# Performance work log

Hardware: AMD Instinct MI355X
Metric: run time of the kernel (lower is better)

Reference implementation:

```python
import jax, jax.numpy as jnp
import numpy as np
from jax import lax

B, H, W, C = 8, 64, 64, 256  # H must equal W (einsum contraction requires it)
CQ = C // 4


def conv2d(x, w, b, dilation=1):
    # x: NHWC, w: HWIO (TF Conv2D layout), padding 'same'
    y = lax.conv_general_dilated(
        x, w, window_strides=(1, 1), padding='SAME',
        rhs_dilation=(dilation, dilation),
        dimension_numbers=('NHWC', 'HWIO', 'NHWC'))
    return y + b


def setup_inputs() -> dict:
    key = jax.random.key(0)
    ks = jax.random.split(key, 16)
    s = 0.05
    inp = {
        'x':   jax.random.normal(ks[0], (B, H, W, C), jnp.float32),
        'wq':  jax.random.normal(ks[1], (1, 1, C, CQ), jnp.float32) * s,
        'bq':  jnp.zeros((CQ,), jnp.float32),
        'wq1': jax.random.normal(ks[2], (3, 3, C, CQ), jnp.float32) * s,
        'bq1': jnp.zeros((CQ,), jnp.float32),
        'wq2': jax.random.normal(ks[3], (3, 3, C, CQ), jnp.float32) * s,
        'bq2': jnp.zeros((CQ,), jnp.float32),
        'wq3': jax.random.normal(ks[4], (3, 3, C, CQ), jnp.float32) * s,
        'bq3': jnp.zeros((CQ,), jnp.float32),
        'wq4': jax.random.normal(ks[5], (1, 1, C, C), jnp.float32) * s,
        'bq4': jnp.zeros((C,), jnp.float32),
        'wk':  jax.random.normal(ks[6], (3, 3, C, C), jnp.float32) * s,
        'bk':  jnp.zeros((C,), jnp.float32),
        'wv':  jax.random.normal(ks[7], (1, 1, C, C), jnp.float32) * s,
        'bv':  jnp.zeros((C,), jnp.float32),
        'gamma': jax.random.normal(ks[8], (1,), jnp.float32) * 0.1,
    }
    return inp


def reference(x, wq, bq, wq1, bq1, wq2, bq2, wq3, bq3, wq4, bq4,
              wk, bk, wv, bv, gamma):
    # multi-scale query branch: 1x1, 3x3, 3x3 dil=3, 3x3 dil=6 -> concat -> 1x1
    q = jnp.concatenate([
        conv2d(x, wq, bq, 1),
        conv2d(x, wq1, bq1, 1),
        conv2d(x, wq2, bq2, 3),
        conv2d(x, wq3, bq3, 6),
    ], axis=-1)
    q = conv2d(q, wq4, bq4, 1)                 # (B,H,W,C)
    # key conv applied twice with the SAME weights (as in the original code)
    k = conv2d(conv2d(x, wk, bk, 1), wk, bk, 1)  # (B,H,W,C)
    v = conv2d(x, wv, bv, 1)                    # (B,H,W,C)

    qT = jnp.transpose(q, (0, 2, 1, 3))         # (B,W,H,C)
    # per-channel spatial contraction; requires H == W
    energy = jnp.einsum('bijc,bkjc->bikc', k, qT)   # (B,H,W,C)
    attention = jax.nn.softmax(energy, axis=-1)     # softmax over CHANNEL axis
    attnT = jnp.transpose(attention, (0, 2, 1, 3))  # (B,W,H,C)
    out = jnp.einsum('bijc,bkjc->bikc', attnT, v)   # (B,W,H,C)
    return gamma * out + x
```

## Files before the change

### kernel.cpp

```cpp
#include <hip/hip_runtime.h>

typedef short  short8 __attribute__((ext_vector_type(8)));
typedef short  sv4    __attribute__((ext_vector_type(4)));
typedef __bf16 bf16x8 __attribute__((ext_vector_type(8)));
typedef float  f32x4  __attribute__((ext_vector_type(4)));

__device__ __forceinline__ float bf2f(short s) {
    unsigned u = ((unsigned)(unsigned short)s) << 16;
    return __builtin_bit_cast(float, u);
}
__device__ __forceinline__ short f2bf(float f) {
    unsigned u = __builtin_bit_cast(unsigned, f);
    u += 0x7fffu + ((u >> 16) & 1u);
    return (short)(u >> 16);
}
__device__ __forceinline__ f32x4 mfma16(short8 a, short8 b, f32x4 c) {
    return __builtin_amdgcn_mfma_f32_16x16x32_bf16(
        __builtin_bit_cast(bf16x8, a), __builtin_bit_cast(bf16x8, b), c, 0, 0, 0);
}
__device__ __forceinline__ void gl16(const short* g, short* l) {
    __builtin_amdgcn_global_load_lds(
        (const __attribute__((address_space(1))) void*)g,
        (__attribute__((address_space(3))) void*)l, 16, 0, 0);
}


__global__ __launch_bounds__(256) void detect_k(const short* x, int* flag)
{
    __shared__ int red[256];
    int t = threadIdx.x;
    int cnt = 0;
    for (int i = t; i < 4096; i += 256) {
        int e = (x[2 * i] >> 7) & 0xFF;
        cnt += (e >= 100 && e <= 140) ? 1 : 0;
    }
    red[t] = cnt; __syncthreads();
    for (int s = 128; s > 0; s >>= 1) { if (t < s) red[t] += red[t + s]; __syncthreads(); }
    if (t == 0) *flag = (red[0] < 3277) ? 1 : 0;
}

__global__ __launch_bounds__(256) void convert_x(const void* x, short* xb, const int* flagp)
{
    int f32 = *flagp;
    size_t i = ((size_t)blockIdx.x * 256 + threadIdx.x) * 8;
    short8 v;
    if (f32) {
        const float* fs = (const float*)x + i;
        f32x4 a = *(const f32x4*)fs;
        f32x4 b = *(const f32x4*)(fs + 4);
#pragma unroll
        for (int l = 0; l < 4; l++) { v[l] = f2bf(a[l]); v[4 + l] = f2bf(b[l]); }
    } else {
        v = *(const short8*)((const short*)x + i);
    }
    *(short8*)(xb + i) = v;
}

struct Ptrs {
    const void *wq, *wq1, *wq2, *wq3, *wq4, *wk, *wv;
    const void *bq, *bq1, *bq2, *bq3, *bq4, *bk, *bv, *gm;
};

__global__ __launch_bounds__(256) void convert_k(Ptrs P, short* wp, short* bb, const int* flagp)
{
    int f32 = *flagp;
    int idx = blockIdx.x * 256 + threadIdx.x;
    if (idx < 1179648) {
        const void* src; int Cout, base;
        if      (idx <   16384) { src = P.wq;  Cout =  64; base = 0; }
        else if (idx <  163840) { src = P.wq1; Cout =  64; base = 16384; }
        else if (idx <  311296) { src = P.wq2; Cout =  64; base = 163840; }
        else if (idx <  458752) { src = P.wq3; Cout =  64; base = 311296; }
        else if (idx <  524288) { src = P.wq4; Cout = 256; base = 458752; }
        else if (idx < 1114112) { src = P.wk;  Cout = 256; base = 524288; }
        else                    { src = P.wv;  Cout = 256; base = 1114112; }
        int rem = idx - base;
        int t   = rem / (Cout * 256);
        int r2  = rem - t * Cout * 256;
        int co  = r2 >> 8;
        int ci  = r2 & 255;
        int si  = (t * 256 + ci) * Cout + co;
        wp[idx] = f32 ? f2bf(((const float*)src)[si]) : ((const short*)src)[si];
    } else if (idx < 1179648 + 1280) {
        int j = idx - 1179648;
        if (j < 1025) {
            const void* src; int off;
            if      (j <   64) { src = P.bq;  off = j; }
            else if (j <  128) { src = P.bq1; off = j - 64; }
            else if (j <  192) { src = P.bq2; off = j - 128; }
            else if (j <  256) { src = P.bq3; off = j - 192; }
            else if (j <  512) { src = P.bq4; off = j - 256; }
            else if (j <  768) { src = P.bk;  off = j - 512; }
            else if (j < 1024) { src = P.bv;  off = j - 768; }
            else               { src = P.gm;  off = 0; }
            bb[j] = f32 ? f2bf(((const float*)src)[off]) : ((const short*)src)[off];
        } else if (j >= 1032) {
            bb[j] = 0;
        }
    }
}

struct CJob {
    const short* src;
    short*       dst;
    const short* wpk;
    const short* bias;
    int Cout;
    int dil;
    int ntaps;
    int coff;
    int outmode;
};
struct CTable { CJob j[6]; int end[6]; };

template<int NA, int NB, int BOFS, int WSTEP>
__device__ __forceinline__ void conv_loop(
    const short* src, const short* wpk, int ntaps, int dil,
    const short* zp, short* Sh,
    int wave, int lr8, int cl, int h0, int b, int nt0, int srcT,
    int m_base, int n_base, int lrow, int pc0, int pc1,
    f32x4 (&acc)[4][4])
{
    const short* abase[NA];
    unsigned     vm[NA];
    const short* bbase[NB];
#pragma unroll
    for (int jj = 0; jj < NA; jj++) {
        int m  = (jj * 4 + wave) * 8 + lr8;
        int hh = srcT ? (m & 63) : (h0 + (m >> 6));
        int ww = srcT ? (h0 + (m >> 6)) : (m & 63);
        abase[jj] = src + (((b * 64 + hh) * 64 + ww) * 256 + cl * 8);
        unsigned msk = 1u;
        if (ntaps == 9) {
            msk = 0u;
#pragma unroll
            for (int t = 0; t < 9; ++t) {
                int tr = (t >= 6) ? 2 : ((t >= 3) ? 1 : 0);
                int dy = (tr - 1) * dil, dx = (t - tr * 3 - 1) * dil;
                bool v = ((unsigned)(hh + dy) < 64u) && ((unsigned)(ww + dx) < 64u);
                msk |= (v ? 1u : 0u) << t;
            }
        }
        vm[jj] = msk;
    }
#pragma unroll
    for (int jj = 0; jj < NB; jj++) {
        int n = (jj * 4 + wave) * 8 + lr8;
        bbase[jj] = wpk + (nt0 + n) * 256 + cl * 8;
    }

    int prevdel = 0;
    for (int t = 0; t < ntaps; ++t) {
        int dy = 0, dx = 0;
        if (ntaps == 9) {
            int tr = (t >= 6) ? 2 : ((t >= 3) ? 1 : 0);
            dy = (tr - 1) * dil;
            dx = (t - tr * 3 - 1) * dil;
        }
        int tdel = (dy * 64 + dx) * 256;
        int step = tdel - prevdel; prevdel = tdel;
        const short* pA[NA];
#pragma unroll
        for (int jj = 0; jj < NA; jj++) {
            abase[jj] += step;
            pA[jj] = ((vm[jj] >> t) & 1u) ? abase[jj] : zp;
        }
#pragma unroll
        for (int s4 = 0; s4 < 4; ++s4) {
#pragma unroll
            for (int jj = 0; jj < NA; jj++)
                gl16(pA[jj] + s4 * 64, Sh + (jj * 4 + wave) * 512);
#pragma unroll
            for (int jj = 0; jj < NB; jj++)
                gl16(bbase[jj] + s4 * 64, Sh + BOFS + (jj * 4 + wave) * 512);
            __syncthreads();
#pragma unroll
            for (int j = 0; j < 2; j++) {
                int pc = j ? pc1 : pc0;
                short8 a4[4], b4[4];
#pragma unroll
                for (int mi = 0; mi < 4; mi++)
                    a4[mi] = *(const short8*)(Sh + (m_base + mi * 16 + lrow) * 64 + pc);
#pragma unroll
                for (int ni = 0; ni < 4; ni++)
                    b4[ni] = *(const short8*)(Sh + BOFS + (n_base + ni * 16 + lrow) * 64 + pc);
#pragma unroll
                for (int mi = 0; mi < 4; mi++)
#pragma unroll
                    for (int ni = 0; ni < 4; ni++)
                        acc[mi][ni] = mfma16(a4[mi], b4[ni], acc[mi][ni]);
            }
            __syncthreads();
        }
#pragma unroll
        for (int jj = 0; jj < NB; jj++) bbase[jj] += WSTEP;
    }
}

__global__ __launch_bounds__(256, 3) void conv_tile(CTable T, const short* zp)
{
    __shared__ short Sh[20480];
    int tid = threadIdx.x;
    int bid = blockIdx.x;
    int ji = 0;
    while (ji < 5 && bid >= T.end[ji]) ji++;
    CJob J = T.j[ji];
    int s0  = ji ? T.end[ji - 1] : 0;
    int seg = T.end[ji] - s0;
    int lb  = bid - s0;
    int g   = (lb & 7) * (seg >> 3) + (lb >> 3);

    int big   = (J.Cout == 256);
    int BM    = big ? 128 : 256;
    int ntile = big ? (g & 1) : 0;
    int Mtile = big ? (g >> 1) : g;
    int p0 = Mtile * BM;
    int b  = p0 >> 12;
    int h0 = (p0 >> 6) & 63;
    int nt0  = ntile * 128;
    int srcT = (J.outmode == 3);

    int wave = tid >> 6, lane = tid & 63;
    int lrow = lane & 15, quad = lane >> 4;
    int m_base = big ? (wave & 1) * 64 : wave * 64;
    int n_base = big ? (wave >> 1) * 64 : 0;

    int lr8 = lane >> 3;
    int cl  = (lane & 7) ^ (lr8 & 7);

    int pc0 = ((quad     ^ (lrow & 7)) * 8);
    int pc1 = (((4 + quad) ^ (lrow & 7)) * 8);

    f32x4 acc[4][4] = {};
    if (big)
        conv_loop<4, 4, 8192, 65536>(J.src, J.wpk, J.ntaps, J.dil, zp, Sh,
                                     wave, lr8, cl, h0, b, nt0, srcT,
                                     m_base, n_base, lrow, pc0, pc1, acc);
    else
        conv_loop<8, 2, 16384, 16384>(J.src, J.wpk, J.ntaps, J.dil, zp, Sh,
                                      wave, lr8, cl, h0, b, nt0, srcT,
                                      m_base, n_base, lrow, pc0, pc1, acc);

    int rq = quad * 4;
#pragma unroll
    for (int ni = 0; ni < 4; ni++) {
        int co = nt0 + n_base + ni * 16 + lrow;
        float bv = bf2f(J.bias[co]);
        if (J.outmode == 0) {
#pragma unroll
            for (int mi = 0; mi < 4; mi++) {
                int pb = p0 + m_base + mi * 16 + rq;
#pragma unroll
                for (int r = 0; r < 4; r++)
                    J.dst[(size_t)(pb + r) * 256 + J.coff + co] = f2bf(acc[mi][ni][r] + bv);
            }
        } else {
            int hw = h0 + (m_base >> 6);
            short* row = J.dst + ((size_t)(b * 256 + co) * 64 + hw) * 64;
#pragma unroll
            for (int mi = 0; mi < 4; mi++) {
                sv4 o;
#pragma unroll
                for (int r = 0; r < 4; r++) o[r] = f2bf(acc[mi][ni][r] + bv);
                *(sv4*)(row + mi * 16 + rq) = o;
            }
        }
    }
}

__global__ __launch_bounds__(256) void energy_mfma(const short* qp, const short* kp, float* Et)
{
    int wid  = threadIdx.x >> 6;
    int lane = threadIdx.x & 63;
    int g = blockIdx.x * 4 + wid;
    int b = g >> 8, c = g & 255;
    int lrow = lane & 15;
    int q8   = (lane >> 4) << 3;
    const short* qb = qp + (size_t)(b * 256 + c) * 4096;
    const short* kb = kp + (size_t)(b * 256 + c) * 4096;

    f32x4 acc[4][4] = {};
#pragma unroll
    for (int ks = 0; ks < 2; ++ks) {
        int j0 = ks * 32 + q8;
        short8 A[4], Bv[4];
#pragma unroll
        for (int mi = 0; mi < 4; mi++)
            A[mi] = *(const short8*)(qb + (size_t)(mi * 16 + lrow) * 64 + j0);
#pragma unroll
        for (int ni = 0; ni < 4; ni++)
            Bv[ni] = *(const short8*)(kb + (size_t)(ni * 16 + lrow) * 64 + j0);
#pragma unroll
        for (int mi = 0; mi < 4; mi++)
#pragma unroll
            for (int ni = 0; ni < 4; ni++)
                acc[mi][ni] = mfma16(A[mi], Bv[ni], acc[mi][ni]);
    }
    int rq = (lane >> 4) * 4;
#pragma unroll
    for (int mi = 0; mi < 4; mi++)
#pragma unroll
        for (int r = 0; r < 4; r++) {
            int w = mi * 16 + rq + r;
            float* row = Et + ((size_t)(b * 256 + c) * 64 + w) * 64;
#pragma unroll
            for (int ni = 0; ni < 4; ni++)
                row[ni * 16 + lrow] = acc[mi][ni][r];
        }
}

__global__ __launch_bounds__(256) void softmax_k(const float* Et, short* att)
{
    __shared__ float S[256 * 33];
    __shared__ float red[256];
    __shared__ float sm[256];
    int t  = threadIdx.x;
    int b  = blockIdx.x >> 7;
    int a  = (blockIdx.x >> 1) & 63;
    int jh = blockIdx.x & 1;

    const float* row = Et + ((size_t)(b * 256 + t) * 64 + a) * 64 + jh * 32;
#pragma unroll
    for (int jj = 0; jj < 32; jj += 4) {
        f32x4 v = *(const f32x4*)(row + jj);
#pragma unroll
        for (int l = 0; l < 4; l++) S[t * 33 + jj + l] = v[l];
    }
    __syncthreads();

    int tj = t & 31, tg = t >> 5;
    float m = -1e30f;
#pragma unroll
    for (int cc = 0; cc < 32; ++cc) m = fmaxf(m, S[(tg * 32 + cc) * 33 + tj]);
    red[t] = m;
    __syncthreads();
    if (tg == 0) {
        float mm = red[tj];
#pragma unroll
        for (int gg = 1; gg < 8; ++gg) mm = fmaxf(mm, red[gg * 32 + tj]);
        red[tj] = mm;
    }
    __syncthreads();
    float M = red[tj];
    float s = 0.f;
#pragma unroll
    for (int cc = 0; cc < 32; ++cc) {
        int id = (tg * 32 + cc) * 33 + tj;
        float e = __expf(S[id] - M);
        S[id] = e; s += e;
    }
    sm[t] = s;
    __syncthreads();
    if (tg == 0) {
        float ss = sm[tj];
#pragma unroll
        for (int gg = 1; gg < 8; ++gg) ss += sm[gg * 32 + tj];
        sm[tj] = 1.0f / ss;
    }
    __syncthreads();

    short* orow = att + ((size_t)(b * 256 + t) * 64 + a) * 64 + jh * 32;
#pragma unroll
    for (int jj = 0; jj < 32; jj += 8) {
        short8 o;
#pragma unroll
        for (int l = 0; l < 8; l++) o[l] = f2bf(S[t * 33 + jj + l] * sm[jj + l]);
        *(short8*)(orow + jj) = o;
    }
}

__global__ __launch_bounds__(256) void out_mfma(const short* vp, const short* att, short* G)
{
    int wid  = threadIdx.x >> 6;
    int lane = threadIdx.x & 63;
    int g = blockIdx.x * 4 + wid;
    int b = g >> 8, c = g & 255;
    int lrow = lane & 15;
    int q8   = (lane >> 4) << 3;
    const short* vb = vp  + (size_t)(b * 256 + c) * 4096;
    const short* ab = att + (size_t)(b * 256 + c) * 4096;

    f32x4 acc[4][4] = {};
#pragma unroll
    for (int ks = 0; ks < 2; ++ks) {
        int j0 = ks * 32 + q8;
        short8 A[4], Bv[4];
#pragma unroll
        for (int mi = 0; mi < 4; mi++)
            A[mi] = *(const short8*)(vb + (size_t)(mi * 16 + lrow) * 64 + j0);
#pragma unroll
        for (int ni = 0; ni < 4; ni++)
            Bv[ni] = *(const short8*)(ab + (size_t)(ni * 16 + lrow) * 64 + j0);
#pragma unroll
        for (int mi = 0; mi < 4; mi++)
#pragma unroll
            for (int ni = 0; ni < 4; ni++)
                acc[mi][ni] = mfma16(A[mi], Bv[ni], acc[mi][ni]);
    }
    int rq = (lane >> 4) * 4;
#pragma unroll
    for (int mi = 0; mi < 4; mi++)
#pragma unroll
        for (int r = 0; r < 4; r++) {
            int d = mi * 16 + rq + r;
            short* row = G + ((size_t)(b * 256 + c) * 64 + d) * 64;
#pragma unroll
            for (int ni = 0; ni < 4; ni++)
                row[ni * 16 + lrow] = f2bf(acc[mi][ni][r]);
        }
}

__global__ __launch_bounds__(256) void final_k(const short* G, const void* x,
                                               const void* gamma, void* out, const int* flagp)
{
    int f32 = *flagp;
    int t = threadIdx.x;
    int b = blockIdx.x >> 6, r = blockIdx.x & 63;
    const short* grow = G + ((size_t)(b * 256 + t) * 64 + r) * 64;
    float gm = f32 ? ((const float*)gamma)[0] : bf2f(((const short*)gamma)[0]);
    size_t obase = ((size_t)(b * 64) * 64 + r) * 256 + t;
    if (f32) {
        const float* xs = (const float*)x;
        float* os = (float*)out;
#pragma unroll
        for (int p8 = 0; p8 < 8; p8++) {
            short8 gv = *(const short8*)(grow + p8 * 8);
#pragma unroll
            for (int l = 0; l < 8; l++) {
                size_t off = obase + (size_t)(p8 * 8 + l) * 16384;
                os[off] = gm * bf2f(gv[l]) + xs[off];
            }
        }
    } else {
        const short* xs = (const short*)x;
        short* os = (short*)out;
#pragma unroll
        for (int p8 = 0; p8 < 8; p8++) {
            short8 gv = *(const short8*)(grow + p8 * 8);
#pragma unroll
            for (int l = 0; l < 8; l++) {
                size_t off = obase + (size_t)(p8 * 8 + l) * 16384;
                os[off] = f2bf(gm * bf2f(gv[l]) + bf2f(xs[off]));
            }
        }
    }
}

extern "C" void kernel_launch(void* const* d_in, const int* in_sizes, int n_in,
                              void* d_out, int out_size, void* d_ws, size_t ws_size,
                              hipStream_t stream)
{
    const void* x   = d_in[0];
    Ptrs P{ d_in[1], d_in[3], d_in[5], d_in[7], d_in[9], d_in[11], d_in[13],
            d_in[2], d_in[4], d_in[6], d_in[8], d_in[10], d_in[12], d_in[14], d_in[15] };

    short* ws   = (short*)d_ws;
    short* qcat = ws;
    short* k1   = ws + 8388608;
    short* qp   = ws + 16777216;
    short* kp   = ws + 25165824;
    short* vp   = ws + 33554432;
    short* wp   = ws + 41943040;
    short* bb   = ws + 43122688;
    int*   flag = (int*)(ws + 43123968);
    short* xb   = qp;
    float* Et   = (float*)d_ws;
    short* att  = qp;
    short* G    = kp;
    const short* zp = bb + 1032;

    detect_k<<<1, 256, 0, stream>>>((const short*)x, flag);
    convert_x<<<4096, 256, 0, stream>>>(x, xb, flag);
    convert_k<<<4613, 256, 0, stream>>>(P, wp, bb, flag);

    CJob j4{ xb, k1,   wp + 524288,  bb + 512, 256, 1, 9, 0,   0 };
    CJob j1{ xb, qcat, wp + 16384,   bb + 64,  64,  1, 9, 64,  0 };
    CJob j2{ xb, qcat, wp + 163840,  bb + 128, 64,  3, 9, 128, 0 };
    CJob j3{ xb, qcat, wp + 311296,  bb + 192, 64,  6, 9, 192, 0 };
    CJob jb{ xb, vp,   wp + 1114112, bb + 768, 256, 1, 1, 0,   2 };
    CJob ja{ xb, qcat, wp + 0,       bb + 0,   64,  1, 1, 0,   0 };
    CTable TA{ { j4, j1, j2, j3, jb, ja }, { 512, 640, 768, 896, 1408, 1536 } };
    conv_tile<<<1536, 256, 0, stream>>>(TA, zp);

    CJob j6{ k1,   kp, wp + 524288, bb + 512, 256, 1, 9, 0, 2 };
    CJob j5{ qcat, qp, wp + 458752, bb + 256, 256, 1, 1, 0, 3 };
    CTable TB{ { j6, j5, j5, j5, j5, j5 }, { 512, 1024, 1024, 1024, 1024, 1024 } };
    conv_tile<<<1024, 256, 0, stream>>>(TB, zp);

    energy_mfma<<<512, 256, 0, stream>>>(qp, kp, Et);
    softmax_k<<<1024, 256, 0, stream>>>(Et, att);
    out_mfma<<<512, 256, 0, stream>>>(vp, att, G);
    final_k<<<512, 256, 0, stream>>>(G, x, d_in[15], d_out, flag);
}
```

Before: 309.6 us.

## Add dedicated 128x256-tile kernel for the 3x3 key convolutions

Moves the two 256-output-channel 3x3 key convolutions out of the generic job-table conv_tile kernel into a new conv8_tile kernel. The new kernel uses 512-thread blocks, 128x256 output tiles and a double-buffered LDS pipeline over 36 K-steps. The larger tile is meant to raise operand reuse per load and MFMA density for the heaviest convolutions. In exchange the remaining jobs run as separate launches (two extra launches in total), and each 256-block conv8 grid is small and may underfill the GPU.

```diff
diff --git a/kernel.cpp b/kernel.cpp
--- a/kernel.cpp
+++ b/kernel.cpp
@@ -100,6 +100,132 @@
     }
 }
 
+struct C8Job {
+    const short* src;
+    short*       dst;
+    const short* wpk;
+    const short* bias;
+    int outmode;
+};
+
+__global__ __launch_bounds__(512, 2) void conv8_tile(C8Job J, const short* zp)
+{
+    __shared__ short Sh[49152];
+    int tid  = threadIdx.x;
+    int wid  = tid >> 6, lane = tid & 63;
+    int bid  = blockIdx.x;
+    int Mtile = (bid & 7) * 32 + (bid >> 3);
+    int p0 = Mtile * 128;
+    int b  = p0 >> 12;
+    int h0 = (p0 >> 6) & 63;
+
+    int lrow = lane & 15, quad = lane >> 4;
+    int lr8  = lane >> 3;
+    int cl   = (lane & 7) ^ (lr8 & 7);
+    int m_base = (wid >> 2) * 64;
+    int n_base = (wid & 3) * 64;
+
+    const short* aroot[2]; unsigned vmask[2];
+#pragma unroll
+    for (int jj = 0; jj < 2; jj++) {
+        int m  = (jj * 8 + wid) * 8 + lr8;
+        int hh = h0 + (m >> 6);
+        int ww = m & 63;
+        aroot[jj] = J.src + (((b * 64 + hh) * 64 + ww) * 256 + cl * 8);
+        unsigned msk = 0;
+#pragma unroll
+        for (int t = 0; t < 9; ++t) {
+            int dy = t / 3 - 1, dx = t % 3 - 1;
+            bool v = ((unsigned)(hh + dy) < 64u) && ((unsigned)(ww + dx) < 64u);
+            msk |= (v ? 1u : 0u) << t;
+        }
+        vmask[jj] = msk;
+    }
+    const short* wroot[4];
+#pragma unroll
+    for (int jj = 0; jj < 4; jj++) {
+        int n = (jj * 8 + wid) * 8 + lr8;
+        wroot[jj] = J.wpk + n * 256 + cl * 8;
+    }
+
+    auto STAGE = [&](int step) {
+        int t = step >> 2, s4 = step & 3;
+        int dy = t / 3 - 1, dx = t % 3 - 1;
+        int tdel = (dy * 64 + dx) * 256 + s4 * 64;
+        short* bufb = Sh + (step & 1) * 24576;
+#pragma unroll
+        for (int jj = 0; jj < 2; jj++) {
+            const short* p = ((vmask[jj] >> t) & 1u) ? (aroot[jj] + tdel) : (zp + s4 * 64);
+            gl16(p, bufb + (jj * 8 + wid) * 512);
+        }
+#pragma unroll
+        for (int jj = 0; jj < 4; jj++)
+            gl16(wroot[jj] + t * 65536 + s4 * 64, bufb + 8192 + (jj * 8 + wid) * 512);
+    };
+
+    f32x4 acc[4][4] = {};
+    STAGE(0);
+    for (int s = 0; s < 36; ++s) {
+        if (s < 35) {
+            STAGE(s + 1);
+            asm volatile("s_waitcnt vmcnt(6)" ::: "memory");
+        } else {
+            asm volatile("s_waitcnt vmcnt(0)" ::: "memory");
+        }
+        __builtin_amdgcn_sched_barrier(0);
+        __builtin_amdgcn_s_barrier();
+        __builtin_amdgcn_sched_barrier(0);
+        const short* bufb = Sh + (s & 1) * 24576;
+#pragma unroll
+        for (int j = 0; j < 2; j++) {
+            int pc = ((j * 4 + quad) ^ (lrow & 7)) * 8;
+            short8 a4[4], b4[4];
+#pragma unroll
+            for (int mi = 0; mi < 4; mi++)
+                a4[mi] = *(const short8*)(bufb + (m_base + mi * 16 + lrow) * 64 + pc);
+#pragma unroll
+            for (int ni = 0; ni < 4; ni++)
+                b4[ni] = *(const short8*)(bufb + 8192 + (n_base + ni * 16 + lrow) * 64 + pc);
+            __builtin_amdgcn_s_setprio(1);
+#pragma unroll
+            for (int mi = 0; mi < 4; mi++)
+#pragma unroll
+                for (int ni = 0; ni < 4; ni++)
+                    acc[mi][ni] = mfma16(a4[mi], b4[ni], acc[mi][ni]);
+            __builtin_amdgcn_s_setprio(0);
+        }
+        __builtin_amdgcn_sched_barrier(0);
+        __builtin_amdgcn_s_barrier();
+        __builtin_amdgcn_sched_barrier(0);
+    }
+
+    int rq = quad * 4;
+#pragma unroll
+    for (int ni = 0; ni < 4; ni++) {
+        int co = n_base + ni * 16 + lrow;
+        float bv = bf2f(J.bias[co]);
+        if (J.outmode == 0) {
+#pragma unroll
+            for (int mi = 0; mi < 4; mi++) {
+                int pb = p0 + m_base + mi * 16 + rq;
+#pragma unroll
+                for (int r = 0; r < 4; r++)
+                    J.dst[(size_t)(pb + r) * 256 + co] = f2bf(acc[mi][ni][r] + bv);
+            }
+        } else {
+            int hw = h0 + (m_base >> 6);
+            short* row = J.dst + ((size_t)(b * 256 + co) * 64 + hw) * 64;
+#pragma unroll
+            for (int mi = 0; mi < 4; mi++) {
+                sv4 o;
+#pragma unroll
+                for (int r = 0; r < 4; r++) o[r] = f2bf(acc[mi][ni][r] + bv);
+                *(sv4*)(row + mi * 16 + rq) = o;
+            }
+        }
+    }
+}
+
 struct CJob {
     const short* src;
     short*       dst;
@@ -473,19 +599,23 @@
     convert_x<<<4096, 256, 0, stream>>>(x, xb, flag);
     convert_k<<<4613, 256, 0, stream>>>(P, wp, bb, flag);
 
-    CJob j4{ xb, k1,   wp + 524288,  bb + 512, 256, 1, 9, 0,   0 };
+    C8Job A8{ xb, k1, wp + 524288, bb + 512, 0 };
+    conv8_tile<<<256, 512, 0, stream>>>(A8, zp);
+
     CJob j1{ xb, qcat, wp + 16384,   bb + 64,  64,  1, 9, 64,  0 };
     CJob j2{ xb, qcat, wp + 163840,  bb + 128, 64,  3, 9, 128, 0 };
     CJob j3{ xb, qcat, wp + 311296,  bb + 192, 64,  6, 9, 192, 0 };
     CJob jb{ xb, vp,   wp + 1114112, bb + 768, 256, 1, 1, 0,   2 };
     CJob ja{ xb, qcat, wp + 0,       bb + 0,   64,  1, 1, 0,   0 };
-    CTable TA{ { j4, j1, j2, j3, jb, ja }, { 512, 640, 768, 896, 1408, 1536 } };
-    conv_tile<<<1536, 256, 0, stream>>>(TA, zp);
-
-    CJob j6{ k1,   kp, wp + 524288, bb + 512, 256, 1, 9, 0, 2 };
+    CTable TA{ { j1, j2, j3, jb, ja, ja }, { 128, 256, 384, 896, 1024, 1024 } };
+    conv_tile<<<1024, 256, 0, stream>>>(TA, zp);
+
+    C8Job B8{ k1, kp, wp + 524288, bb + 512, 2 };
+    conv8_tile<<<256, 512, 0, stream>>>(B8, zp);
+
     CJob j5{ qcat, qp, wp + 458752, bb + 256, 256, 1, 1, 0, 3 };
-    CTable TB{ { j6, j5, j5, j5, j5, j5 }, { 512, 1024, 1024, 1024, 1024, 1024 } };
-    conv_tile<<<1024, 256, 0, stream>>>(TB, zp);
+    CTable TB{ { j5, j5, j5, j5, j5, j5 }, { 512, 512, 512, 512, 512, 512 } };
+    conv_tile<<<512, 256, 0, stream>>>(TB, zp);
 
     energy_mfma<<<512, 256, 0, stream>>>(qp, kp, Et);
     softmax_k<<<1024, 256, 0, stream>>>(Et, att);
```

Result: slower. 330.1 us (+6.6%).

## Fuse attention-output GEMM with residual epilogue and tile weight transpose

Applied to the files above, without the earlier changes.

The out_mfma and final_k kernels are merged into a single out_final kernel. Eight channels per block are staged through shared memory so the gamma-scaled residual add writes channel-contiguous vector stores directly to the output, which removes the intermediate G buffer round-trip and the strided scalar stores. The weight conversion kernel now transposes through a 64x64 LDS tile, so both its reads and writes are coalesced. The trade-offs are fewer, larger blocks in out_final (256 blocks of 512 threads) and extra barriers per output sub-tile.

```diff
diff --git a/kernel.cpp b/kernel.cpp
--- a/kernel.cpp
+++ b/kernel.cpp
@@ -64,38 +64,50 @@
 __global__ __launch_bounds__(256) void convert_k(Ptrs P, short* wp, short* bb, const int* flagp)
 {
     int f32 = *flagp;
-    int idx = blockIdx.x * 256 + threadIdx.x;
-    if (idx < 1179648) {
-        const void* src; int Cout, base;
-        if      (idx <   16384) { src = P.wq;  Cout =  64; base = 0; }
-        else if (idx <  163840) { src = P.wq1; Cout =  64; base = 16384; }
-        else if (idx <  311296) { src = P.wq2; Cout =  64; base = 163840; }
-        else if (idx <  458752) { src = P.wq3; Cout =  64; base = 311296; }
-        else if (idx <  524288) { src = P.wq4; Cout = 256; base = 458752; }
-        else if (idx < 1114112) { src = P.wk;  Cout = 256; base = 524288; }
-        else                    { src = P.wv;  Cout = 256; base = 1114112; }
-        int rem = idx - base;
-        int t   = rem / (Cout * 256);
-        int r2  = rem - t * Cout * 256;
-        int co  = r2 >> 8;
-        int ci  = r2 & 255;
-        int si  = (t * 256 + ci) * Cout + co;
-        wp[idx] = f32 ? f2bf(((const float*)src)[si]) : ((const short*)src)[si];
-    } else if (idx < 1179648 + 1280) {
-        int j = idx - 1179648;
-        if (j < 1025) {
-            const void* src; int off;
-            if      (j <   64) { src = P.bq;  off = j; }
-            else if (j <  128) { src = P.bq1; off = j - 64; }
-            else if (j <  192) { src = P.bq2; off = j - 128; }
-            else if (j <  256) { src = P.bq3; off = j - 192; }
-            else if (j <  512) { src = P.bq4; off = j - 256; }
-            else if (j <  768) { src = P.bk;  off = j - 512; }
-            else if (j < 1024) { src = P.bv;  off = j - 768; }
-            else               { src = P.gm;  off = 0; }
-            bb[j] = f32 ? f2bf(((const float*)src)[off]) : ((const short*)src)[off];
-        } else if (j >= 1032) {
-            bb[j] = 0;
+    int bid = blockIdx.x;
+    int tid = threadIdx.x;
+    if (bid < 288) {
+        __shared__ short T[64][66];
+        const void* src; int Cout, dbase, lb;
+        if      (bid <   4) { src = P.wq;  Cout =  64; dbase = 0;       lb = bid; }
+        else if (bid <  40) { src = P.wq1; Cout =  64; dbase = 16384;   lb = bid - 4; }
+        else if (bid <  76) { src = P.wq2; Cout =  64; dbase = 163840;  lb = bid - 40; }
+        else if (bid < 112) { src = P.wq3; Cout =  64; dbase = 311296;  lb = bid - 76; }
+        else if (bid < 128) { src = P.wq4; Cout = 256; dbase = 458752;  lb = bid - 112; }
+        else if (bid < 272) { src = P.wk;  Cout = 256; dbase = 524288;  lb = bid - 128; }
+        else                { src = P.wv;  Cout = 256; dbase = 1114112; lb = bid - 272; }
+        int t, ci0, co0;
+        if (Cout == 64) { t = lb >> 2; ci0 = (lb & 3) * 64; co0 = 0; }
+        else            { t = lb >> 4; ci0 = ((lb >> 2) & 3) * 64; co0 = (lb & 3) * 64; }
+        int rrow = tid >> 6, ccol = tid & 63;
+#pragma unroll
+        for (int r = 0; r < 16; ++r) {
+            int cir = r * 4 + rrow;
+            long si = (long)(t * 256 + ci0 + cir) * Cout + co0 + ccol;
+            T[cir][ccol] = f32 ? f2bf(((const float*)src)[si]) : ((const short*)src)[si];
+        }
+        __syncthreads();
+#pragma unroll
+        for (int r = 0; r < 16; ++r) {
+            int cow = r * 4 + rrow;
+            wp[dbase + (t * Cout + co0 + cow) * 256 + ci0 + ccol] = T[ccol][cow];
+        }
+    } else {
+        for (int j = tid; j < 1280; j += 256) {
+            if (j < 1025) {
+                const void* src; int off;
+                if      (j <   64) { src = P.bq;  off = j; }
+                else if (j <  128) { src = P.bq1; off = j - 64; }
+                else if (j <  192) { src = P.bq2; off = j - 128; }
+                else if (j <  256) { src = P.bq3; off = j - 192; }
+                else if (j <  512) { src = P.bq4; off = j - 256; }
+                else if (j <  768) { src = P.bk;  off = j - 512; }
+                else if (j < 1024) { src = P.bv;  off = j - 768; }
+                else               { src = P.gm;  off = 0; }
+                bb[j] = f32 ? f2bf(((const float*)src)[off]) : ((const short*)src)[off];
+            } else if (j >= 1032) {
+                bb[j] = 0;
+            }
         }
     }
 }
@@ -369,14 +381,19 @@
     }
 }
 
-__global__ __launch_bounds__(256) void out_mfma(const short* vp, const short* att, short* G)
-{
-    int wid  = threadIdx.x >> 6;
-    int lane = threadIdx.x & 63;
-    int g = blockIdx.x * 4 + wid;
-    int b = g >> 8, c = g & 255;
-    int lrow = lane & 15;
-    int q8   = (lane >> 4) << 3;
+__global__ __launch_bounds__(512) void out_final(const short* vp, const short* att,
+                                                 const void* x, const void* gamma,
+                                                 void* out, const int* flagp)
+{
+    __shared__ float S[8 * 16 * 66];
+    int f32 = *flagp;
+    int tid = threadIdx.x;
+    int wid = tid >> 6, lane = tid & 63;
+    int b  = blockIdx.x & 7;
+    int c0 = (blockIdx.x >> 3) * 8;
+    int c  = c0 + wid;
+    int lrow = lane & 15, quad = lane >> 4;
+    int q8 = quad << 3;
     const short* vb = vp  + (size_t)(b * 256 + c) * 4096;
     const short* ab = att + (size_t)(b * 256 + c) * 4096;
 
@@ -397,52 +414,48 @@
             for (int ni = 0; ni < 4; ni++)
                 acc[mi][ni] = mfma16(A[mi], Bv[ni], acc[mi][ni]);
     }
-    int rq = (lane >> 4) * 4;
-#pragma unroll
-    for (int mi = 0; mi < 4; mi++)
-#pragma unroll
-        for (int r = 0; r < 4; r++) {
-            int d = mi * 16 + rq + r;
-            short* row = G + ((size_t)(b * 256 + c) * 64 + d) * 64;
-#pragma unroll
-            for (int ni = 0; ni < 4; ni++)
-                row[ni * 16 + lrow] = f2bf(acc[mi][ni][r]);
-        }
-}
-
-__global__ __launch_bounds__(256) void final_k(const short* G, const void* x,
-                                               const void* gamma, void* out, const int* flagp)
-{
-    int f32 = *flagp;
-    int t = threadIdx.x;
-    int b = blockIdx.x >> 6, r = blockIdx.x & 63;
-    const short* grow = G + ((size_t)(b * 256 + t) * 64 + r) * 64;
+
     float gm = f32 ? ((const float*)gamma)[0] : bf2f(((const short*)gamma)[0]);
-    size_t obase = ((size_t)(b * 64) * 64 + r) * 256 + t;
-    if (f32) {
-        const float* xs = (const float*)x;
-        float* os = (float*)out;
-#pragma unroll
-        for (int p8 = 0; p8 < 8; p8++) {
-            short8 gv = *(const short8*)(grow + p8 * 8);
-#pragma unroll
-            for (int l = 0; l < 8; l++) {
-                size_t off = obase + (size_t)(p8 * 8 + l) * 16384;
-                os[off] = gm * bf2f(gv[l]) + xs[off];
+    int rq = quad * 4;
+#pragma unroll
+    for (int mi = 0; mi < 4; mi++) {
+#pragma unroll
+        for (int ni = 0; ni < 4; ni++)
+#pragma unroll
+            for (int r = 0; r < 4; r++)
+                S[(wid * 16 + rq + r) * 66 + ni * 16 + lrow] = acc[mi][ni][r];
+        __syncthreads();
+#pragma unroll
+        for (int it = 0; it < 2; ++it) {
+            int idx = it * 512 + tid;
+            int dp = idx >> 6;
+            int p  = idx & 63;
+            int dg = mi * 16 + dp;
+            size_t off = ((size_t)((b * 64 + p) * 64 + dg)) * 256 + c0;
+            if (f32) {
+                const float* xs = (const float*)x + off;
+                float* os = (float*)out + off;
+                f32x4 xv0 = *(const f32x4*)xs;
+                f32x4 xv1 = *(const f32x4*)(xs + 4);
+                f32x4 o0, o1;
+#pragma unroll
+                for (int l = 0; l < 4; l++) {
+                    o0[l] = gm * S[((l    ) * 16 + dp) * 66 + p] + xv0[l];
+                    o1[l] = gm * S[((l + 4) * 16 + dp) * 66 + p] + xv1[l];
+                }
+                *(f32x4*)os = o0;
+                *(f32x4*)(os + 4) = o1;
+            } else {
+                const short* xs = (const short*)x + off;
+                short* os = (short*)out + off;
+                short8 xv = *(const short8*)xs, o;
+#pragma unroll
+                for (int l = 0; l < 8; l++)
+                    o[l] = f2bf(gm * S[(l * 16 + dp) * 66 + p] + bf2f(xv[l]));
+                *(short8*)os = o;
             }
         }
-    } else {
-        const short* xs = (const short*)x;
-        short* os = (short*)out;
-#pragma unroll
-        for (int p8 = 0; p8 < 8; p8++) {
-            short8 gv = *(const short8*)(grow + p8 * 8);
-#pragma unroll
-            for (int l = 0; l < 8; l++) {
-                size_t off = obase + (size_t)(p8 * 8 + l) * 16384;
-                os[off] = f2bf(gm * bf2f(gv[l]) + bf2f(xs[off]));
-            }
-        }
+        __syncthreads();
     }
 }
 
@@ -466,12 +479,11 @@
     short* xb   = qp;
     float* Et   = (float*)d_ws;
     short* att  = qp;
-    short* G    = kp;
     const short* zp = bb + 1032;
 
     detect_k<<<1, 256, 0, stream>>>((const short*)x, flag);
     convert_x<<<4096, 256, 0, stream>>>(x, xb, flag);
-    convert_k<<<4613, 256, 0, stream>>>(P, wp, bb, flag);
+    convert_k<<<289, 256, 0, stream>>>(P, wp, bb, flag);
 
     CJob j4{ xb, k1,   wp + 524288,  bb + 512, 256, 1, 9, 0,   0 };
     CJob j1{ xb, qcat, wp + 16384,   bb + 64,  64,  1, 9, 64,  0 };
@@ -489,6 +501,5 @@
 
     energy_mfma<<<512, 256, 0, stream>>>(qp, kp, Et);
     softmax_k<<<1024, 256, 0, stream>>>(Et, att);
-    out_mfma<<<512, 256, 0, stream>>>(vp, att, G);
-    final_k<<<512, 256, 0, stream>>>(G, x, d_in[15], d_out, flag);
-}
+    out_final<<<256, 512, 0, stream>>>(vp, att, x, d_in[15], d_out, flag);
+}
```

Result: no change. 314.0 us (+1.4%).
